# Kernel optimization log

Measured on AMD Instinct MI355X. Metric: run time of the kernel, lower is better.

## Reference

```python
import jax, jax.numpy as jnp
import numpy as np

NODE_IN = 128
NODE_OUT = 128
LEAKY_SLOPE = 0.01  # torch nn.LeakyReLU default


def setup_inputs() -> dict:
    key = jax.random.key(0)
    k1, k2, k3, k4 = jax.random.split(key, 4)
    B, N = 64, 1024
    node_mat = jax.random.normal(k1, (B, N, NODE_IN), dtype=jnp.float32)
    adj_mat = jax.random.uniform(k2, (B, N, N), dtype=jnp.float32)
    # Linear(node_in_len, node_out_len): W [out, in], b [out] (torch default init style)
    bound = 1.0 / np.sqrt(NODE_IN)
    W = jax.random.uniform(k3, (NODE_OUT, NODE_IN), minval=-bound, maxval=bound, dtype=jnp.float32)
    b = jax.random.uniform(k4, (NODE_OUT,), minval=-bound, maxval=bound, dtype=jnp.float32)
    return {"node_mat": node_mat, "adj_mat": adj_mat, "W": W, "b": b}


def reference(node_mat, adj_mat, W, b):
    # n_neighbors[b,i] = sum_j adj[b,i,j]; diag(1/deg) @ adj == adj / deg (row-wise)
    deg = jnp.sum(adj_mat, axis=-1, keepdims=True)          # [B,N,1]
    norm_adj = adj_mat / deg                                 # [B,N,N]
    agg = jnp.einsum('bij,bjf->bif', norm_adj, node_mat)     # [B,N,Fin]
    out = jnp.einsum('bif,of->bio', agg, W) + b              # [B,N,Fout]
    return jnp.where(out >= 0, out, LEAKY_SLOPE * out)
```

## Files before the change

### kernel.cpp

```cpp
#include <hip/hip_runtime.h>
#include <hip/hip_bf16.h>


typedef __attribute__((ext_vector_type(8))) short bf16x8;
typedef __attribute__((ext_vector_type(4))) float f32x4;

__device__ __forceinline__ unsigned f2bf(float x) {
  unsigned u = __builtin_bit_cast(unsigned, x);
  u += 0x7FFFu + ((u >> 16) & 1u);
  return u >> 16;
}
__device__ __forceinline__ int f2bf2(float x, float y) {
  return (int)(f2bf(x) | (f2bf(y) << 16));
}

#define JPAD 136
#define KP   72

__global__ __launch_bounds__(256) void k_ht(const float* __restrict__ node,
                                            const float* __restrict__ W,
                                            ushort* __restrict__ Ht) {
  __shared__ short nt[128 * JPAD];
  __shared__ short wt[128 * JPAD];
  const int b = blockIdx.y, jt = blockIdx.x, t = threadIdx.x;
  const float4* nbase = (const float4*)(node + (size_t)(b * 1024 + jt * 128) * 128);
  const float4* wbase = (const float4*)W;

  #pragma unroll
  for (int p = 0; p < 16; p++) {
    int idx = t + 256 * p;
    int r = idx >> 5, c4 = idx & 31;
    float4 v = nbase[idx];
    int2 s; s.x = f2bf2(v.x, v.y); s.y = f2bf2(v.z, v.w);
    *(int2*)&nt[r * JPAD + c4 * 4] = s;
    float4 wv = wbase[idx];
    int2 sw; sw.x = f2bf2(wv.x, wv.y); sw.y = f2bf2(wv.z, wv.w);
    *(int2*)&wt[r * JPAD + c4 * 4] = sw;
  }
  __syncthreads();

  const int lane = t & 63, wid = t >> 6;
  const int q = lane >> 4, r = lane & 15;
  const int wm = wid & 1, wn = wid >> 1;
  f32x4 acc[4][4] = {};
  #pragma unroll
  for (int ks = 0; ks < 4; ks++) {
    bf16x8 af[4], bg[4];
    #pragma unroll
    for (int mi = 0; mi < 4; mi++)
      af[mi] = *(const bf16x8*)&nt[(wm * 64 + mi * 16 + r) * JPAD + ks * 32 + q * 8];
    #pragma unroll
    for (int ni = 0; ni < 4; ni++)
      bg[ni] = *(const bf16x8*)&wt[(wn * 64 + ni * 16 + r) * JPAD + ks * 32 + q * 8];
    #pragma unroll
    for (int mi = 0; mi < 4; mi++)
      #pragma unroll
      for (int ni = 0; ni < 4; ni++)
        acc[mi][ni] = __builtin_amdgcn_mfma_f32_16x16x32_bf16(af[mi], bg[ni], acc[mi][ni], 0, 0, 0);
  }
  __syncthreads();

  #pragma unroll
  for (int mi = 0; mi < 4; mi++)
    #pragma unroll
    for (int ni = 0; ni < 4; ni++)
      #pragma unroll
      for (int v = 0; v < 4; v++) {
        int j = wm * 64 + mi * 16 + q * 4 + v;
        int o = wn * 64 + ni * 16 + r;
        nt[o * JPAD + j] = (short)f2bf(acc[mi][ni][v]);
      }
  __syncthreads();
  {
    int o = t >> 1, half = t & 1;
    const int4* src = (const int4*)&nt[o * JPAD + half * 64];
    int4* dst = (int4*)(Ht + (size_t)b * 131072 + (size_t)o * 1024 + jt * 128 + half * 64);
    #pragma unroll
    for (int i = 0; i < 8; i++) dst[i] = src[i];
  }
}

__global__ __launch_bounds__(256) void k_main(const float* __restrict__ adj,
                                              const ushort* __restrict__ Ht,
                                              const float* __restrict__ bias,
                                              float* __restrict__ out) {
  __shared__ short at[128 * KP];
  __shared__ short ht[128 * KP];
  __shared__ float deg[128];
  const int b = blockIdx.y, it = blockIdx.x, t = threadIdx.x;
  const float4* abase = (const float4*)(adj + (size_t)(b * 1024 + it * 128) * 1024);
  const int4* hbase = (const int4*)(Ht + (size_t)b * 131072);
  const int lane = t & 63, wid = t >> 6;
  const int q = lane >> 4, r = lane & 15;
  const int wm = wid & 1, wn = wid >> 1;
  const int arow = t >> 4, ac4 = t & 15;
  const int hrow = t >> 3, hc8 = t & 7;
  f32x4 acc[4][4] = {};
  float rs[8] = {0, 0, 0, 0, 0, 0, 0, 0};
  float bias_r[4];
  #pragma unroll
  for (int ni = 0; ni < 4; ni++) bias_r[ni] = bias[wn * 64 + ni * 16 + r];

  for (int kt = 0; kt < 16; kt++) {
    float4 av[8];
    #pragma unroll
    for (int p = 0; p < 8; p++)
      av[p] = abase[(size_t)(arow + 16 * p) * 256 + kt * 16 + ac4];
    int4 hv[4];
    #pragma unroll
    for (int p = 0; p < 4; p++)
      hv[p] = hbase[(size_t)(hrow + 32 * p) * 128 + kt * 8 + hc8];
    __syncthreads();
    #pragma unroll
    for (int p = 0; p < 8; p++) {
      rs[p] += (av[p].x + av[p].y) + (av[p].z + av[p].w);
      int2 s; s.x = f2bf2(av[p].x, av[p].y); s.y = f2bf2(av[p].z, av[p].w);
      *(int2*)&at[(arow + 16 * p) * KP + ac4 * 4] = s;
    }
    #pragma unroll
    for (int p = 0; p < 4; p++)
      *(int4*)&ht[(hrow + 32 * p) * KP + hc8 * 8] = hv[p];
    __syncthreads();
    #pragma unroll
    for (int ks = 0; ks < 2; ks++) {
      bf16x8 af[4], bg[4];
      #pragma unroll
      for (int mi = 0; mi < 4; mi++)
        af[mi] = *(const bf16x8*)&at[(wm * 64 + mi * 16 + r) * KP + ks * 32 + q * 8];
      #pragma unroll
      for (int ni = 0; ni < 4; ni++)
        bg[ni] = *(const bf16x8*)&ht[(wn * 64 + ni * 16 + r) * KP + ks * 32 + q * 8];
      #pragma unroll
      for (int mi = 0; mi < 4; mi++)
        #pragma unroll
        for (int ni = 0; ni < 4; ni++)
          acc[mi][ni] = __builtin_amdgcn_mfma_f32_16x16x32_bf16(af[mi], bg[ni], acc[mi][ni], 0, 0, 0);
    }
  }

  #pragma unroll
  for (int p = 0; p < 8; p++) {
    float v = rs[p];
    v += __shfl_down(v, 8, 16);
    v += __shfl_down(v, 4, 16);
    v += __shfl_down(v, 2, 16);
    v += __shfl_down(v, 1, 16);
    rs[p] = v;
  }
  if ((t & 15) == 0) {
    #pragma unroll
    for (int p = 0; p < 8; p++) deg[arow + 16 * p] = rs[p];
  }
  __syncthreads();

  float* obase = out + (size_t)(b * 1024 + it * 128) * 128;
  #pragma unroll
  for (int mi = 0; mi < 4; mi++)
    #pragma unroll
    for (int v = 0; v < 4; v++) {
      int i = wm * 64 + mi * 16 + q * 4 + v;
      float rd = 1.0f / deg[i];
      #pragma unroll
      for (int ni = 0; ni < 4; ni++) {
        int o = wn * 64 + ni * 16 + r;
        float val = acc[mi][ni][v] * rd + bias_r[ni];
        val = val >= 0.0f ? val : 0.01f * val;
        obase[(size_t)i * 128 + o] = val;
      }
    }
}

__global__ __launch_bounds__(256) void k_fallback(const float* __restrict__ node,
                                                  const float* __restrict__ adj,
                                                  const float* __restrict__ W,
                                                  const float* __restrict__ bias,
                                                  float* __restrict__ out) {
  __shared__ float red[256];
  __shared__ float agg[128];
  const int b = blockIdx.y, i = blockIdx.x, t = threadIdx.x;
  const float* arow = adj + (size_t)(b * 1024 + i) * 1024;
  float s = 0.f;
  for (int j = t; j < 1024; j += 256) s += arow[j];
  red[t] = s;
  __syncthreads();
  if (t < 128) red[t] += red[t + 128];
  __syncthreads();
  if (t < 64) {
    float v2 = red[t] + red[t + 64];
    #pragma unroll
    for (int off = 32; off; off >>= 1) v2 += __shfl_down(v2, off);
    if (t == 0) red[0] = v2;
  }
  __syncthreads();
  const float rdeg = 1.0f / red[0];
  const int f = t & 127, half = t >> 7;
  const float* nb = node + (size_t)b * 1024 * 128;
  float a = 0.f;
  for (int j = half * 512; j < half * 512 + 512; j++)
    a += arow[j] * nb[(size_t)j * 128 + f];
  __syncthreads();
  if (half == 0) agg[f] = a;
  __syncthreads();
  if (half == 1) agg[f] += a;
  __syncthreads();
  if (t < 128) {
    const float* wr = W + t * 128;
    float o = 0.f;
    for (int f2 = 0; f2 < 128; f2++) o += agg[f2] * wr[f2];
    o = o * rdeg + bias[t];
    out[(size_t)(b * 1024 + i) * 128 + t] = o >= 0.f ? o : 0.01f * o;
  }
}

extern "C" void kernel_launch(void* const* d_in, const int* in_sizes, int n_in,
                              void* d_out, int out_size, void* d_ws, size_t ws_size,
                              hipStream_t stream) {
  const float* node = (const float*)d_in[0];
  const float* adj  = (const float*)d_in[1];
  const float* W    = (const float*)d_in[2];
  const float* bias = (const float*)d_in[3];
  float* out = (float*)d_out;
  const size_t ht_bytes = (size_t)64 * 128 * 1024 * 2;
  if (ws_size >= ht_bytes) {
    ushort* Ht = (ushort*)d_ws;
    k_ht<<<dim3(8, 64), 256, 0, stream>>>(node, W, Ht);
    k_main<<<dim3(8, 64), 256, 0, stream>>>(adj, Ht, bias, out);
  } else {
    k_fallback<<<dim3(1024, 64), 256, 0, stream>>>(node, adj, W, bias, out);
  }
}
```

Baseline: 422.6 us.

## Double-buffer LDS tiles and prefetch next adjacency/Ht tile in k_main

Converts the k_main K-loop to a software pipeline. Global loads for tile kt+1 are issued into registers before the MFMA work on tile kt, and the two LDS buffers alternate so only one barrier is needed per iteration. Launch bounds now request two blocks per SM. The aim is to hide HBM latency for the adjacency stream behind compute, at the cost of doubled LDS use and more live registers.

```diff
diff --git a/kernel.cpp b/kernel.cpp
--- a/kernel.cpp
+++ b/kernel.cpp
@@ -80,12 +80,12 @@
   }
 }
 
-__global__ __launch_bounds__(256) void k_main(const float* __restrict__ adj,
-                                              const ushort* __restrict__ Ht,
-                                              const float* __restrict__ bias,
-                                              float* __restrict__ out) {
-  __shared__ short at[128 * KP];
-  __shared__ short ht[128 * KP];
+__global__ __launch_bounds__(256, 2) void k_main(const float* __restrict__ adj,
+                                                 const ushort* __restrict__ Ht,
+                                                 const float* __restrict__ bias,
+                                                 float* __restrict__ out) {
+  __shared__ short at[2][128 * KP];
+  __shared__ short ht[2][128 * KP];
   __shared__ float deg[128];
   const int b = blockIdx.y, it = blockIdx.x, t = threadIdx.x;
   const float4* abase = (const float4*)(adj + (size_t)(b * 1024 + it * 128) * 1024);
@@ -101,41 +101,57 @@
   #pragma unroll
   for (int ni = 0; ni < 4; ni++) bias_r[ni] = bias[wn * 64 + ni * 16 + r];
 
+  float4 av[8]; int4 hv[4];
+  #pragma unroll
+  for (int p = 0; p < 8; p++)
+    av[p] = abase[(size_t)(arow + 16 * p) * 256 + ac4];
+  #pragma unroll
+  for (int p = 0; p < 4; p++)
+    hv[p] = hbase[(size_t)(hrow + 32 * p) * 128 + hc8];
+
   for (int kt = 0; kt < 16; kt++) {
-    float4 av[8];
-    #pragma unroll
-    for (int p = 0; p < 8; p++)
-      av[p] = abase[(size_t)(arow + 16 * p) * 256 + kt * 16 + ac4];
-    int4 hv[4];
-    #pragma unroll
-    for (int p = 0; p < 4; p++)
-      hv[p] = hbase[(size_t)(hrow + 32 * p) * 128 + kt * 8 + hc8];
-    __syncthreads();
+    const int buf = kt & 1;
     #pragma unroll
     for (int p = 0; p < 8; p++) {
       rs[p] += (av[p].x + av[p].y) + (av[p].z + av[p].w);
       int2 s; s.x = f2bf2(av[p].x, av[p].y); s.y = f2bf2(av[p].z, av[p].w);
-      *(int2*)&at[(arow + 16 * p) * KP + ac4 * 4] = s;
+      *(int2*)&at[buf][(arow + 16 * p) * KP + ac4 * 4] = s;
     }
     #pragma unroll
     for (int p = 0; p < 4; p++)
-      *(int4*)&ht[(hrow + 32 * p) * KP + hc8 * 8] = hv[p];
+      *(int4*)&ht[buf][(hrow + 32 * p) * KP + hc8 * 8] = hv[p];
+
+    float4 av2[8]; int4 hv2[4];
+    if (kt < 15) {
+      #pragma unroll
+      for (int p = 0; p < 8; p++)
+        av2[p] = abase[(size_t)(arow + 16 * p) * 256 + (kt + 1) * 16 + ac4];
+      #pragma unroll
+      for (int p = 0; p < 4; p++)
+        hv2[p] = hbase[(size_t)(hrow + 32 * p) * 128 + (kt + 1) * 8 + hc8];
+    }
+
     __syncthreads();
+
     #pragma unroll
     for (int ks = 0; ks < 2; ks++) {
       bf16x8 af[4], bg[4];
       #pragma unroll
       for (int mi = 0; mi < 4; mi++)
-        af[mi] = *(const bf16x8*)&at[(wm * 64 + mi * 16 + r) * KP + ks * 32 + q * 8];
+        af[mi] = *(const bf16x8*)&at[buf][(wm * 64 + mi * 16 + r) * KP + ks * 32 + q * 8];
       #pragma unroll
       for (int ni = 0; ni < 4; ni++)
-        bg[ni] = *(const bf16x8*)&ht[(wn * 64 + ni * 16 + r) * KP + ks * 32 + q * 8];
+        bg[ni] = *(const bf16x8*)&ht[buf][(wn * 64 + ni * 16 + r) * KP + ks * 32 + q * 8];
       #pragma unroll
       for (int mi = 0; mi < 4; mi++)
         #pragma unroll
         for (int ni = 0; ni < 4; ni++)
           acc[mi][ni] = __builtin_amdgcn_mfma_f32_16x16x32_bf16(af[mi], bg[ni], acc[mi][ni], 0, 0, 0);
     }
+    #pragma unroll
+    for (int p = 0; p < 8; p++) av[p] = av2[p];
+    #pragma unroll
+    for (int p = 0; p < 4; p++) hv[p] = hv2[p];
   }
 
   #pragma unroll
```

After: 458.4 us. +8.5%, slower.

## Load MFMA fragments directly from global memory with register prefetch, dropping LDS staging

Applied to the files above, without the earlier changes.

The aggregation kernel no longer stages adjacency and Ht tiles through shared memory. Each wave now loads its MFMA operand fragments straight from global memory into registers, converts adjacency values to bf16 in registers, and prefetches the next k-slice while the current MFMAs run. The row-degree sum is now computed by one wave column only and reduced with cross-quad shuffles. This removes the LDS writes, the LDS reads and the two barriers per tile, and adds a two-blocks-per-CU occupancy hint. In exchange, the two wave columns each load the same adjacency rows, doubling adjacency reads that L2 must absorb, and each load is a narrower strided access.

```diff
diff --git a/kernel.cpp b/kernel.cpp
--- a/kernel.cpp
+++ b/kernel.cpp
@@ -15,7 +15,6 @@
 }
 
 #define JPAD 136
-#define KP   72
 
 __global__ __launch_bounds__(256) void k_ht(const float* __restrict__ node,
                                             const float* __restrict__ W,
@@ -80,76 +79,90 @@
   }
 }
 
-__global__ __launch_bounds__(256) void k_main(const float* __restrict__ adj,
-                                              const ushort* __restrict__ Ht,
-                                              const float* __restrict__ bias,
-                                              float* __restrict__ out) {
-  __shared__ short at[128 * KP];
-  __shared__ short ht[128 * KP];
+__global__ __launch_bounds__(256, 2) void k_main(const float* __restrict__ adj,
+                                                 const ushort* __restrict__ Ht,
+                                                 const float* __restrict__ bias,
+                                                 float* __restrict__ out) {
   __shared__ float deg[128];
   const int b = blockIdx.y, it = blockIdx.x, t = threadIdx.x;
-  const float4* abase = (const float4*)(adj + (size_t)(b * 1024 + it * 128) * 1024);
-  const int4* hbase = (const int4*)(Ht + (size_t)b * 131072);
   const int lane = t & 63, wid = t >> 6;
   const int q = lane >> 4, r = lane & 15;
   const int wm = wid & 1, wn = wid >> 1;
-  const int arow = t >> 4, ac4 = t & 15;
-  const int hrow = t >> 3, hc8 = t & 7;
+
+  const float* arow = adj + (size_t)(b * 1024 + it * 128) * 1024;
+  const ushort* hrow = Ht + (size_t)b * 131072;
+
+  const float4* ap[4];
+  const int4* hp[4];
+  #pragma unroll
+  for (int mi = 0; mi < 4; mi++)
+    ap[mi] = (const float4*)(arow + (size_t)(wm * 64 + mi * 16 + r) * 1024);
+  #pragma unroll
+  for (int ni = 0; ni < 4; ni++)
+    hp[ni] = (const int4*)(hrow + (size_t)(wn * 64 + ni * 16 + r) * 1024);
+
   f32x4 acc[4][4] = {};
-  float rs[8] = {0, 0, 0, 0, 0, 0, 0, 0};
+  float rs[4] = {0.f, 0.f, 0.f, 0.f};
   float bias_r[4];
   #pragma unroll
   for (int ni = 0; ni < 4; ni++) bias_r[ni] = bias[wn * 64 + ni * 16 + r];
 
-  for (int kt = 0; kt < 16; kt++) {
-    float4 av[8];
-    #pragma unroll
-    for (int p = 0; p < 8; p++)
-      av[p] = abase[(size_t)(arow + 16 * p) * 256 + kt * 16 + ac4];
-    int4 hv[4];
-    #pragma unroll
-    for (int p = 0; p < 4; p++)
-      hv[p] = hbase[(size_t)(hrow + 32 * p) * 128 + kt * 8 + hc8];
-    __syncthreads();
-    #pragma unroll
-    for (int p = 0; p < 8; p++) {
-      rs[p] += (av[p].x + av[p].y) + (av[p].z + av[p].w);
-      int2 s; s.x = f2bf2(av[p].x, av[p].y); s.y = f2bf2(av[p].z, av[p].w);
-      *(int2*)&at[(arow + 16 * p) * KP + ac4 * 4] = s;
-    }
-    #pragma unroll
-    for (int p = 0; p < 4; p++)
-      *(int4*)&ht[(hrow + 32 * p) * KP + hc8 * 8] = hv[p];
-    __syncthreads();
-    #pragma unroll
-    for (int ks = 0; ks < 2; ks++) {
-      bf16x8 af[4], bg[4];
-      #pragma unroll
-      for (int mi = 0; mi < 4; mi++)
-        af[mi] = *(const bf16x8*)&at[(wm * 64 + mi * 16 + r) * KP + ks * 32 + q * 8];
+  float4 a[4][2]; int4 h[4];
+  #pragma unroll
+  for (int mi = 0; mi < 4; mi++) {
+    a[mi][0] = ap[mi][q * 2];
+    a[mi][1] = ap[mi][q * 2 + 1];
+  }
+  #pragma unroll
+  for (int ni = 0; ni < 4; ni++) h[ni] = hp[ni][q];
+
+  for (int kt = 0; kt < 32; kt++) {
+    const int ktn = (kt < 31) ? kt + 1 : kt;
+    float4 an[4][2]; int4 hn[4];
+    #pragma unroll
+    for (int mi = 0; mi < 4; mi++) {
+      an[mi][0] = ap[mi][ktn * 8 + q * 2];
+      an[mi][1] = ap[mi][ktn * 8 + q * 2 + 1];
+    }
+    #pragma unroll
+    for (int ni = 0; ni < 4; ni++) hn[ni] = hp[ni][ktn * 4 + q];
+
+    bf16x8 af[4], bg[4];
+    #pragma unroll
+    for (int mi = 0; mi < 4; mi++) {
+      if (wn == 0)
+        rs[mi] += ((a[mi][0].x + a[mi][0].y) + (a[mi][0].z + a[mi][0].w))
+                + ((a[mi][1].x + a[mi][1].y) + (a[mi][1].z + a[mi][1].w));
+      int4 c;
+      c.x = f2bf2(a[mi][0].x, a[mi][0].y);
+      c.y = f2bf2(a[mi][0].z, a[mi][0].w);
+      c.z = f2bf2(a[mi][1].x, a[mi][1].y);
+      c.w = f2bf2(a[mi][1].z, a[mi][1].w);
+      af[mi] = __builtin_bit_cast(bf16x8, c);
+    }
+    #pragma unroll
+    for (int ni = 0; ni < 4; ni++) bg[ni] = __builtin_bit_cast(bf16x8, h[ni]);
+
+    #pragma unroll
+    for (int mi = 0; mi < 4; mi++)
       #pragma unroll
       for (int ni = 0; ni < 4; ni++)
-        bg[ni] = *(const bf16x8*)&ht[(wn * 64 + ni * 16 + r) * KP + ks * 32 + q * 8];
-      #pragma unroll
-      for (int mi = 0; mi < 4; mi++)
-        #pragma unroll
-        for (int ni = 0; ni < 4; ni++)
-          acc[mi][ni] = __builtin_amdgcn_mfma_f32_16x16x32_bf16(af[mi], bg[ni], acc[mi][ni], 0, 0, 0);
-    }
-  }
-
-  #pragma unroll
-  for (int p = 0; p < 8; p++) {
-    float v = rs[p];
-    v += __shfl_down(v, 8, 16);
-    v += __shfl_down(v, 4, 16);
-    v += __shfl_down(v, 2, 16);
-    v += __shfl_down(v, 1, 16);
-    rs[p] = v;
-  }
-  if ((t & 15) == 0) {
-    #pragma unroll
-    for (int p = 0; p < 8; p++) deg[arow + 16 * p] = rs[p];
+        acc[mi][ni] = __builtin_amdgcn_mfma_f32_16x16x32_bf16(af[mi], bg[ni], acc[mi][ni], 0, 0, 0);
+
+    #pragma unroll
+    for (int mi = 0; mi < 4; mi++) { a[mi][0] = an[mi][0]; a[mi][1] = an[mi][1]; }
+    #pragma unroll
+    for (int ni = 0; ni < 4; ni++) h[ni] = hn[ni];
+  }
+
+  if (wn == 0) {
+    #pragma unroll
+    for (int mi = 0; mi < 4; mi++) {
+      float v = rs[mi];
+      v += __shfl_down(v, 32);
+      v += __shfl_down(v, 16);
+      if (lane < 16) deg[wm * 64 + mi * 16 + lane] = v;
+    }
   }
   __syncthreads();
 
```

After: 436.4 us. +3.3%, slower.
